# Performance work log

Measured on AMD Instinct MI355X. Metric: run time of the kernel, lower is better.

## Reference

```python
import jax, jax.numpy as jnp
import numpy as np

B, N, F, R, H = 64, 128, 128, 64, 256
L = 3           # number of DTNN layers (hidden_dim=[256,256,256])
FC = 256        # fc_hidden_dim[0]
OUT = 1
SCALE = 0.05


def setup_inputs() -> dict:
    key = jax.random.key(0)
    ks = jax.random.split(key, 12)
    inp = {
        "x": jax.random.normal(ks[0], (B, N, F), dtype=jnp.float32),
        # RBF-expanded pairwise distances are nonnegative
        "distance": jax.random.uniform(ks[1], (B, N, N, R), dtype=jnp.float32),
        # stacked per-layer params (all layers share shapes since hidden dims equal)
        "Wcf_w": jax.random.normal(ks[2], (L, H, F), dtype=jnp.float32) * SCALE,
        "Wcf_b": jax.random.normal(ks[3], (L, H), dtype=jnp.float32) * SCALE,
        "Wdf_w": jax.random.normal(ks[4], (L, H, R), dtype=jnp.float32) * SCALE,
        "Wdf_b": jax.random.normal(ks[5], (L, H), dtype=jnp.float32) * SCALE,
        "Wfc_w": jax.random.normal(ks[6], (L, F, H), dtype=jnp.float32) * SCALE,  # no bias
        "fc0_w": jax.random.normal(ks[7], (FC, F), dtype=jnp.float32) * SCALE,
        "fc0_b": jax.random.normal(ks[8], (FC,), dtype=jnp.float32) * SCALE,
        "out_w": jax.random.normal(ks[9], (OUT, FC), dtype=jnp.float32) * SCALE,
        "out_b": jax.random.normal(ks[10], (OUT,), dtype=jnp.float32) * SCALE,
    }
    return inp


def reference(x, distance, Wcf_w, Wcf_b, Wdf_w, Wdf_b, Wfc_w, fc0_w, fc0_b, out_w, out_b):
    # Original per-layer math:
    #   msg_i = sum_j Wfc( Wcf(x_i) * Wdf(d_ij) )
    # Since Wcf(x_i) is independent of j and all maps are linear, this equals
    #   Wfc( Wcf(x_i) * (sum_j d_ij) @ Wdf_w^T + N * Wdf_b ),
    # which avoids materializing the (B,N,N,H) grid while computing identical math.
    n = x.shape[1]
    d_sum = jnp.sum(distance, axis=2)  # (B, N, R)
    for l in range(Wcf_w.shape[0]):
        cf = jnp.einsum('bnf,hf->bnh', x, Wcf_w[l]) + Wcf_b[l]            # (B,N,H)
        df = jnp.einsum('bnr,hr->bnh', d_sum, Wdf_w[l]) + n * Wdf_b[l]    # (B,N,H)
        h = jnp.einsum('bnh,fh->bnf', cf * df, Wfc_w[l])                  # (B,N,F)
        x = h + jnp.tanh(h)                                                # residual-tanh
    g = jnp.sum(x, axis=1)                     # sum pooling over nodes -> (B,F)
    g = g @ fc0_w.T + fc0_b                    # (B,FC)
    return g @ out_w.T + out_b                 # (B,OUT)
```

## Files before the change

### kernel.cpp

```cpp
#include <hip/hip_runtime.h>
#include <math.h>

#define B_ 64
#define N_ 128
#define F_ 128
#define R_ 64
#define H_ 256
#define L_ 3
#define M_ (B_*N_)

#define DS_PAD 72
#define X_PAD 136
#define P_PAD 264

#define PREPW_NBLK 48
#define COMB_BID   48
#define DSUM_BID0  49

typedef short bf16x8 __attribute__((ext_vector_type(8)));
typedef float f32x4 __attribute__((ext_vector_type(4)));

__device__ __forceinline__ unsigned short f2bf(float f) {
    unsigned int u = __float_as_uint(f);
    u += 0x7FFF + ((u >> 16) & 1);
    return (unsigned short)(u >> 16);
}

__device__ __forceinline__ float tanh_fast(float h) {
    float a = fabsf(h);
    float e = __expf(-2.0f * a);
    float t = (1.0f - e) * __builtin_amdgcn_rcpf(1.0f + e);
    return copysignf(t, h);
}

__global__ __launch_bounds__(256)
void dsum_prep_kernel(const float* __restrict__ dist,
                      const float* __restrict__ wcf,
                      const float* __restrict__ wdf,
                      const float* __restrict__ wfc,
                      const float* __restrict__ fc0_w, const float* __restrict__ fc0_b,
                      const float* __restrict__ out_w, const float* __restrict__ out_b,
                      unsigned short* __restrict__ wcfb,
                      unsigned short* __restrict__ wdfb,
                      unsigned short* __restrict__ wfcb,
                      float* __restrict__ wcomb,
                      unsigned short* __restrict__ dsumb,
                      float* __restrict__ out) {
    const int bid = blockIdx.x;
    const int t   = threadIdx.x;

    if (bid < PREPW_NBLK) {
        const int NCF = L_*H_*F_/4;
        const int NDF = L_*H_*R_/4;
        const int NFC = L_*F_*H_/4;
        const int total = NCF + NDF + NFC;
        for (int i = bid*256 + t; i < total; i += PREPW_NBLK*256) {
            const float4* src; unsigned short* dst; int k;
            if (i < NCF)           { src = (const float4*)wcf; dst = wcfb; k = i; }
            else if (i < NCF+NDF)  { src = (const float4*)wdf; dst = wdfb; k = i-NCF; }
            else                   { src = (const float4*)wfc; dst = wfcb; k = i-NCF-NDF; }
            float4 v = src[k];
            ushort4 o; o.x=f2bf(v.x); o.y=f2bf(v.y); o.z=f2bf(v.z); o.w=f2bf(v.w);
            ((ushort4*)dst)[k] = o;
        }
        return;
    }
    if (bid == COMB_BID) {
        if (t < 128) {
            float s = 0.f;
            #pragma unroll 8
            for (int c = 0; c < 256; ++c) s += out_w[c] * fc0_w[c*128 + t];
            wcomb[t] = s;
        } else if (t < 192) {
            float bb = out_b[0];
            #pragma unroll 8
            for (int c = 0; c < 256; ++c) bb += out_w[c] * fc0_b[c];
            out[t - 128] = bb;
        }
        return;
    }

    const int row = bid - DSUM_BID0;
    const float4* src = (const float4*)(dist + (size_t)row * (N_*R_));
    const int q = t & 15, jg = t >> 4;
    float4 a = make_float4(0.f,0.f,0.f,0.f);
    #pragma unroll
    for (int j0 = 0; j0 < N_; j0 += 16) {
        float4 v = src[(j0 + jg)*16 + q];
        a.x += v.x; a.y += v.y; a.z += v.z; a.w += v.w;
    }
    __shared__ float4 sh[256];
    sh[t] = a;
    __syncthreads();
    if (t < 16) {
        float4 s = sh[t];
        for (int g = 1; g < 16; ++g) {
            float4 v = sh[t + 16*g];
            s.x += v.x; s.y += v.y; s.z += v.z; s.w += v.w;
        }
        ushort4 o; o.x=f2bf(s.x); o.y=f2bf(s.y); o.z=f2bf(s.z); o.w=f2bf(s.w);
        ((ushort4*)(dsumb + (size_t)row * R_))[t] = o;
    }
}

__global__ __launch_bounds__(512)
void layers_kernel(const float* __restrict__ x,
                   const unsigned short* __restrict__ dsumb,
                   const unsigned short* __restrict__ wcfb,
                   const unsigned short* __restrict__ wdfb,
                   const unsigned short* __restrict__ wfcb,
                   const float* __restrict__ bcf,
                   const float* __restrict__ bdf,
                   const float* __restrict__ wcomb,
                   float* __restrict__ out) {
    __shared__ __align__(16) unsigned short ds_lds[32][DS_PAD];
    __shared__ __align__(16) unsigned short x_lds[32][X_PAD];
    __shared__ __align__(16) unsigned short p_lds[32][P_PAD];

    const int blk  = blockIdx.x;
    const int t    = threadIdx.x;
    const int w    = t >> 6, lane = t & 63;
    const int lr   = lane & 15, lg = lane >> 4;
    const int mh   = w & 1,  nq = w >> 1;

    {
        const int row16 = t >> 4, q = t & 15;
        const float4* xs = (const float4*)(x + (size_t)(blk*32 + row16)*F_ + q*8);
        float4 xv0 = xs[0], xv1 = xs[1];
        bf16x8 xb;
        xb[0]=f2bf(xv0.x); xb[1]=f2bf(xv0.y); xb[2]=f2bf(xv0.z); xb[3]=f2bf(xv0.w);
        xb[4]=f2bf(xv1.x); xb[5]=f2bf(xv1.y); xb[6]=f2bf(xv1.z); xb[7]=f2bf(xv1.w);
        *(bf16x8*)&x_lds[row16][q*8] = xb;

        if (t < 256) {
            const uint4* dsrc = (const uint4*)(dsumb + (size_t)(blk*32 + (t>>3))*R_);
            uint4 v = dsrc[t & 7];
            *(uint4*)&ds_lds[t>>3][(t&7)*8] = v;
        }
    }
    __syncthreads();

    float pool_acc = 0.f;

    #pragma unroll 1
    for (int l = 0; l < L_; ++l) {
        const unsigned short* wcf = wcfb + l*H_*F_;
        const unsigned short* wdf = wdfb + l*H_*R_;
        const unsigned short* wfc = wfcb + l*F_*H_;

        bf16x8 xa[4], da[2];
        #pragma unroll
        for (int kc = 0; kc < 4; ++kc)
            xa[kc] = *(const bf16x8*)&x_lds[mh*16 + lr][kc*32 + lg*8];
        #pragma unroll
        for (int kc = 0; kc < 2; ++kc)
            da[kc] = *(const bf16x8*)&ds_lds[mh*16 + lr][kc*32 + lg*8];

        #pragma unroll
        for (int nt = 0; nt < 4; ++nt) {
            const int ncol = nq*64 + nt*16 + lr;
            f32x4 acf = {0.f,0.f,0.f,0.f}, adf = {0.f,0.f,0.f,0.f};
            #pragma unroll
            for (int kc = 0; kc < 4; ++kc) {
                bf16x8 b = *(const bf16x8*)(wcf + (size_t)ncol*F_ + kc*32 + lg*8);
                acf = __builtin_amdgcn_mfma_f32_16x16x32_bf16(xa[kc], b, acf, 0, 0, 0);
            }
            #pragma unroll
            for (int kc = 0; kc < 2; ++kc) {
                bf16x8 b = *(const bf16x8*)(wdf + (size_t)ncol*R_ + kc*32 + lg*8);
                adf = __builtin_amdgcn_mfma_f32_16x16x32_bf16(da[kc], b, adf, 0, 0, 0);
            }
            const float bc = bcf[l*H_ + ncol];
            const float bd = bdf[l*H_ + ncol] * 128.0f;
            #pragma unroll
            for (int j = 0; j < 4; ++j) {
                float p = (acf[j] + bc) * (adf[j] + bd);
                p_lds[mh*16 + lg*4 + j][ncol] = f2bf(p);
            }
        }
        __syncthreads();

        f32x4 ah[2] = {{0,0,0,0},{0,0,0,0}};
        #pragma unroll
        for (int kc = 0; kc < 8; ++kc) {
            bf16x8 ap = *(const bf16x8*)&p_lds[mh*16 + lr][kc*32 + lg*8];
            #pragma unroll
            for (int ct = 0; ct < 2; ++ct) {
                const int ncol = nq*32 + ct*16 + lr;
                bf16x8 b = *(const bf16x8*)(wfc + (size_t)ncol*H_ + kc*32 + lg*8);
                ah[ct] = __builtin_amdgcn_mfma_f32_16x16x32_bf16(ap, b, ah[ct], 0, 0, 0);
            }
        }
        __syncthreads();

        if (l < L_-1) {
            #pragma unroll
            for (int ct = 0; ct < 2; ++ct) {
                #pragma unroll
                for (int j = 0; j < 4; ++j) {
                    float h = ah[ct][j];
                    float xo = h + tanh_fast(h);
                    x_lds[mh*16 + lg*4 + j][nq*32 + ct*16 + lr] = f2bf(xo);
                }
            }
            __syncthreads();
        } else {
            #pragma unroll
            for (int ct = 0; ct < 2; ++ct) {
                const float wc = wcomb[nq*32 + ct*16 + lr];
                #pragma unroll
                for (int j = 0; j < 4; ++j) {
                    float h = ah[ct][j];
                    float xo = h + tanh_fast(h);
                    pool_acc += xo * wc;
                }
            }
        }
    }

    float* red = (float*)&p_lds[0][0];
    red[t] = pool_acc;
    __syncthreads();
    #pragma unroll
    for (int s = 256; s > 0; s >>= 1) {
        if (t < s) red[t] += red[t + s];
        __syncthreads();
    }
    if (t == 0) atomicAdd(&out[blk >> 2], red[0]);
}

extern "C" void kernel_launch(void* const* d_in, const int* in_sizes, int n_in,
                              void* d_out, int out_size, void* d_ws, size_t ws_size,
                              hipStream_t stream) {
    const float* x     = (const float*)d_in[0];
    const float* dist  = (const float*)d_in[1];
    const float* wcf_w = (const float*)d_in[2];
    const float* wcf_b = (const float*)d_in[3];
    const float* wdf_w = (const float*)d_in[4];
    const float* wdf_b = (const float*)d_in[5];
    const float* wfc_w = (const float*)d_in[6];
    const float* fc0_w = (const float*)d_in[7];
    const float* fc0_b = (const float*)d_in[8];
    const float* out_w = (const float*)d_in[9];
    const float* out_b = (const float*)d_in[10];
    float* out = (float*)d_out;

    char* ws = (char*)d_ws;
    unsigned short* wcfb  = (unsigned short*)(ws);
    unsigned short* wdfb  = (unsigned short*)(ws + 196608u);
    unsigned short* wfcb  = (unsigned short*)(ws + 294912u);
    float*          wcomb = (float*)(ws + 491520u);
    unsigned short* dsumb = (unsigned short*)(ws + 492032u);

    dsum_prep_kernel<<<DSUM_BID0 + M_, 256, 0, stream>>>(
        dist, wcf_w, wdf_w, wfc_w, fc0_w, fc0_b, out_w, out_b,
        wcfb, wdfb, wfcb, wcomb, dsumb, out);

    layers_kernel<<<M_/32, 512, 0, stream>>>(x, dsumb, wcfb, wdfb, wfcb,
                                             wcf_b, wdf_b, wcomb, out);
}
```

Baseline: 78.31 us.

## Fuse distance summation into layers kernel with 16-row blocks

Moves the per-row reduction over the 256 MB distance tensor out of the prep kernel and into the main layers kernel. Each of the 8 waves now sums two rows with shuffles, and the block tile shrinks from 32 to 16 rows so 512 blocks are launched. This removes the bf16 dsum round trip through global memory and lets the dominant distance read overlap with the MFMA layer compute. The cost is that weights are re-read by twice as many blocks, and the prep kernel now only converts weights, so it is tiny.

Result: slower. 88.86 us (+13.5%).

```diff
diff --git a/kernel.cpp b/kernel.cpp
--- a/kernel.cpp
+++ b/kernel.cpp
@@ -8,6 +8,8 @@
 #define H_ 256
 #define L_ 3
 #define M_ (B_*N_)
+#define RPB 16
+#define NBLK (M_/RPB)
 
 #define DS_PAD 72
 #define X_PAD 136
@@ -15,7 +17,6 @@
 
 #define PREPW_NBLK 48
 #define COMB_BID   48
-#define DSUM_BID0  49
 
 typedef short bf16x8 __attribute__((ext_vector_type(8)));
 typedef float f32x4 __attribute__((ext_vector_type(4)));
@@ -34,18 +35,16 @@
 }
 
 __global__ __launch_bounds__(256)
-void dsum_prep_kernel(const float* __restrict__ dist,
-                      const float* __restrict__ wcf,
-                      const float* __restrict__ wdf,
-                      const float* __restrict__ wfc,
-                      const float* __restrict__ fc0_w, const float* __restrict__ fc0_b,
-                      const float* __restrict__ out_w, const float* __restrict__ out_b,
-                      unsigned short* __restrict__ wcfb,
-                      unsigned short* __restrict__ wdfb,
-                      unsigned short* __restrict__ wfcb,
-                      float* __restrict__ wcomb,
-                      unsigned short* __restrict__ dsumb,
-                      float* __restrict__ out) {
+void prep_kernel(const float* __restrict__ wcf,
+                 const float* __restrict__ wdf,
+                 const float* __restrict__ wfc,
+                 const float* __restrict__ fc0_w, const float* __restrict__ fc0_b,
+                 const float* __restrict__ out_w, const float* __restrict__ out_b,
+                 unsigned short* __restrict__ wcfb,
+                 unsigned short* __restrict__ wdfb,
+                 unsigned short* __restrict__ wfcb,
+                 float* __restrict__ wcomb,
+                 float* __restrict__ out) {
     const int bid = blockIdx.x;
     const int t   = threadIdx.x;
 
@@ -65,77 +64,76 @@
         }
         return;
     }
-    if (bid == COMB_BID) {
-        if (t < 128) {
-            float s = 0.f;
-            #pragma unroll 8
-            for (int c = 0; c < 256; ++c) s += out_w[c] * fc0_w[c*128 + t];
-            wcomb[t] = s;
-        } else if (t < 192) {
-            float bb = out_b[0];
-            #pragma unroll 8
-            for (int c = 0; c < 256; ++c) bb += out_w[c] * fc0_b[c];
-            out[t - 128] = bb;
-        }
-        return;
-    }
-
-    const int row = bid - DSUM_BID0;
-    const float4* src = (const float4*)(dist + (size_t)row * (N_*R_));
-    const int q = t & 15, jg = t >> 4;
-    float4 a = make_float4(0.f,0.f,0.f,0.f);
-    #pragma unroll
-    for (int j0 = 0; j0 < N_; j0 += 16) {
-        float4 v = src[(j0 + jg)*16 + q];
-        a.x += v.x; a.y += v.y; a.z += v.z; a.w += v.w;
-    }
-    __shared__ float4 sh[256];
-    sh[t] = a;
-    __syncthreads();
-    if (t < 16) {
-        float4 s = sh[t];
-        for (int g = 1; g < 16; ++g) {
-            float4 v = sh[t + 16*g];
-            s.x += v.x; s.y += v.y; s.z += v.z; s.w += v.w;
-        }
-        ushort4 o; o.x=f2bf(s.x); o.y=f2bf(s.y); o.z=f2bf(s.z); o.w=f2bf(s.w);
-        ((ushort4*)(dsumb + (size_t)row * R_))[t] = o;
-    }
-}
-
-__global__ __launch_bounds__(512)
-void layers_kernel(const float* __restrict__ x,
-                   const unsigned short* __restrict__ dsumb,
-                   const unsigned short* __restrict__ wcfb,
-                   const unsigned short* __restrict__ wdfb,
-                   const unsigned short* __restrict__ wfcb,
-                   const float* __restrict__ bcf,
-                   const float* __restrict__ bdf,
-                   const float* __restrict__ wcomb,
-                   float* __restrict__ out) {
-    __shared__ __align__(16) unsigned short ds_lds[32][DS_PAD];
-    __shared__ __align__(16) unsigned short x_lds[32][X_PAD];
-    __shared__ __align__(16) unsigned short p_lds[32][P_PAD];
+    if (t < 128) {
+        float s = 0.f;
+        #pragma unroll 8
+        for (int c = 0; c < 256; ++c) s += out_w[c] * fc0_w[c*128 + t];
+        wcomb[t] = s;
+    } else if (t < 192) {
+        float bb = out_b[0];
+        #pragma unroll 8
+        for (int c = 0; c < 256; ++c) bb += out_w[c] * fc0_b[c];
+        out[t - 128] = bb;
+    }
+}
+
+__global__ __launch_bounds__(512, 4)
+void mega_kernel(const float* __restrict__ x,
+                 const float* __restrict__ dist,
+                 const unsigned short* __restrict__ wcfb,
+                 const unsigned short* __restrict__ wdfb,
+                 const unsigned short* __restrict__ wfcb,
+                 const float* __restrict__ biascf,
+                 const float* __restrict__ biasdf,
+                 const float* __restrict__ wcomb,
+                 float* __restrict__ out) {
+    __shared__ __align__(16) unsigned short ds_lds[RPB][DS_PAD];
+    __shared__ __align__(16) unsigned short x_lds[RPB][X_PAD];
+    __shared__ __align__(16) unsigned short p_lds[RPB][P_PAD];
 
     const int blk  = blockIdx.x;
     const int t    = threadIdx.x;
     const int w    = t >> 6, lane = t & 63;
     const int lr   = lane & 15, lg = lane >> 4;
-    const int mh   = w & 1,  nq = w >> 1;
 
     {
-        const int row16 = t >> 4, q = t & 15;
-        const float4* xs = (const float4*)(x + (size_t)(blk*32 + row16)*F_ + q*8);
-        float4 xv0 = xs[0], xv1 = xs[1];
-        bf16x8 xb;
-        xb[0]=f2bf(xv0.x); xb[1]=f2bf(xv0.y); xb[2]=f2bf(xv0.z); xb[3]=f2bf(xv0.w);
-        xb[4]=f2bf(xv1.x); xb[5]=f2bf(xv1.y); xb[6]=f2bf(xv1.z); xb[7]=f2bf(xv1.w);
-        *(bf16x8*)&x_lds[row16][q*8] = xb;
-
-        if (t < 256) {
-            const uint4* dsrc = (const uint4*)(dsumb + (size_t)(blk*32 + (t>>3))*R_);
-            uint4 v = dsrc[t & 7];
-            *(uint4*)&ds_lds[t>>3][(t&7)*8] = v;
+        const int row = t >> 5, c = t & 31;
+        float4 v = ((const float4*)(x + (size_t)(blk*RPB + row)*F_))[c];
+        ushort4 o; o.x=f2bf(v.x); o.y=f2bf(v.y); o.z=f2bf(v.z); o.w=f2bf(v.w);
+        *(ushort4*)&x_lds[row][c*4] = o;
+    }
+
+    {
+        const float4* s0 = (const float4*)(dist + (size_t)(blk*RPB + w*2) * (N_*R_));
+        const float4* s1 = s0 + (N_*R_/4);
+        float4 a00 = {0,0,0,0}, a01 = {0,0,0,0}, a10 = {0,0,0,0}, a11 = {0,0,0,0};
+        #pragma unroll 4
+        for (int ii = 0; ii < 32; ii += 2) {
+            float4 v0 = s0[ii*64 + lane];
+            float4 v1 = s0[(ii+1)*64 + lane];
+            float4 v2 = s1[ii*64 + lane];
+            float4 v3 = s1[(ii+1)*64 + lane];
+            a00.x+=v0.x; a00.y+=v0.y; a00.z+=v0.z; a00.w+=v0.w;
+            a01.x+=v1.x; a01.y+=v1.y; a01.z+=v1.z; a01.w+=v1.w;
+            a10.x+=v2.x; a10.y+=v2.y; a10.z+=v2.z; a10.w+=v2.w;
+            a11.x+=v3.x; a11.y+=v3.y; a11.z+=v3.z; a11.w+=v3.w;
+        }
+        float4 a0, a1;
+        a0.x=a00.x+a01.x; a0.y=a00.y+a01.y; a0.z=a00.z+a01.z; a0.w=a00.w+a01.w;
+        a1.x=a10.x+a11.x; a1.y=a10.y+a11.y; a1.z=a10.z+a11.z; a1.w=a10.w+a11.w;
+        a0.x += __shfl_xor(a0.x, 16); a0.y += __shfl_xor(a0.y, 16);
+        a0.z += __shfl_xor(a0.z, 16); a0.w += __shfl_xor(a0.w, 16);
+        a0.x += __shfl_xor(a0.x, 32); a0.y += __shfl_xor(a0.y, 32);
+        a0.z += __shfl_xor(a0.z, 32); a0.w += __shfl_xor(a0.w, 32);
+        a1.x += __shfl_xor(a1.x, 16); a1.y += __shfl_xor(a1.y, 16);
+        a1.z += __shfl_xor(a1.z, 16); a1.w += __shfl_xor(a1.w, 16);
+        a1.x += __shfl_xor(a1.x, 32); a1.y += __shfl_xor(a1.y, 32);
+        a1.z += __shfl_xor(a1.z, 32); a1.w += __shfl_xor(a1.w, 32);
+        if (lane < 16) {
+            ushort4 o0; o0.x=f2bf(a0.x); o0.y=f2bf(a0.y); o0.z=f2bf(a0.z); o0.w=f2bf(a0.w);
+            *(ushort4*)&ds_lds[w*2][lane*4] = o0;
+            ushort4 o1; o1.x=f2bf(a1.x); o1.y=f2bf(a1.y); o1.z=f2bf(a1.z); o1.w=f2bf(a1.w);
+            *(ushort4*)&ds_lds[w*2+1][lane*4] = o1;
         }
     }
     __syncthreads();
@@ -151,14 +149,14 @@
         bf16x8 xa[4], da[2];
         #pragma unroll
         for (int kc = 0; kc < 4; ++kc)
-            xa[kc] = *(const bf16x8*)&x_lds[mh*16 + lr][kc*32 + lg*8];
+            xa[kc] = *(const bf16x8*)&x_lds[lr][kc*32 + lg*8];
         #pragma unroll
         for (int kc = 0; kc < 2; ++kc)
-            da[kc] = *(const bf16x8*)&ds_lds[mh*16 + lr][kc*32 + lg*8];
-
-        #pragma unroll
-        for (int nt = 0; nt < 4; ++nt) {
-            const int ncol = nq*64 + nt*16 + lr;
+            da[kc] = *(const bf16x8*)&ds_lds[lr][kc*32 + lg*8];
+
+        #pragma unroll
+        for (int nt = 0; nt < 2; ++nt) {
+            const int ncol = w*32 + nt*16 + lr;
             f32x4 acf = {0.f,0.f,0.f,0.f}, adf = {0.f,0.f,0.f,0.f};
             #pragma unroll
             for (int kc = 0; kc < 4; ++kc) {
@@ -170,50 +168,40 @@
                 bf16x8 b = *(const bf16x8*)(wdf + (size_t)ncol*R_ + kc*32 + lg*8);
                 adf = __builtin_amdgcn_mfma_f32_16x16x32_bf16(da[kc], b, adf, 0, 0, 0);
             }
-            const float bc = bcf[l*H_ + ncol];
-            const float bd = bdf[l*H_ + ncol] * 128.0f;
+            const float bc = biascf[l*H_ + ncol];
+            const float bd = biasdf[l*H_ + ncol] * 128.0f;
             #pragma unroll
             for (int j = 0; j < 4; ++j) {
                 float p = (acf[j] + bc) * (adf[j] + bd);
-                p_lds[mh*16 + lg*4 + j][ncol] = f2bf(p);
+                p_lds[lg*4 + j][ncol] = f2bf(p);
             }
         }
         __syncthreads();
 
-        f32x4 ah[2] = {{0,0,0,0},{0,0,0,0}};
+        const int ncol2 = w*16 + lr;
+        f32x4 ah = {0.f,0.f,0.f,0.f};
         #pragma unroll
         for (int kc = 0; kc < 8; ++kc) {
-            bf16x8 ap = *(const bf16x8*)&p_lds[mh*16 + lr][kc*32 + lg*8];
-            #pragma unroll
-            for (int ct = 0; ct < 2; ++ct) {
-                const int ncol = nq*32 + ct*16 + lr;
-                bf16x8 b = *(const bf16x8*)(wfc + (size_t)ncol*H_ + kc*32 + lg*8);
-                ah[ct] = __builtin_amdgcn_mfma_f32_16x16x32_bf16(ap, b, ah[ct], 0, 0, 0);
-            }
+            bf16x8 b  = *(const bf16x8*)(wfc + (size_t)ncol2*H_ + kc*32 + lg*8);
+            bf16x8 ap = *(const bf16x8*)&p_lds[lr][kc*32 + lg*8];
+            ah = __builtin_amdgcn_mfma_f32_16x16x32_bf16(ap, b, ah, 0, 0, 0);
         }
         __syncthreads();
 
         if (l < L_-1) {
             #pragma unroll
-            for (int ct = 0; ct < 2; ++ct) {
-                #pragma unroll
-                for (int j = 0; j < 4; ++j) {
-                    float h = ah[ct][j];
-                    float xo = h + tanh_fast(h);
-                    x_lds[mh*16 + lg*4 + j][nq*32 + ct*16 + lr] = f2bf(xo);
-                }
+            for (int j = 0; j < 4; ++j) {
+                float h = ah[j];
+                float xo = h + tanh_fast(h);
+                x_lds[lg*4 + j][ncol2] = f2bf(xo);
             }
             __syncthreads();
         } else {
-            #pragma unroll
-            for (int ct = 0; ct < 2; ++ct) {
-                const float wc = wcomb[nq*32 + ct*16 + lr];
-                #pragma unroll
-                for (int j = 0; j < 4; ++j) {
-                    float h = ah[ct][j];
-                    float xo = h + tanh_fast(h);
-                    pool_acc += xo * wc;
-                }
+            const float wc = wcomb[ncol2];
+            #pragma unroll
+            for (int j = 0; j < 4; ++j) {
+                float h = ah[j];
+                pool_acc += (h + tanh_fast(h)) * wc;
             }
         }
     }
@@ -226,7 +214,7 @@
         if (t < s) red[t] += red[t + s];
         __syncthreads();
     }
-    if (t == 0) atomicAdd(&out[blk >> 2], red[0]);
+    if (t == 0) atomicAdd(&out[blk >> 3], red[0]);
 }
 
 extern "C" void kernel_launch(void* const* d_in, const int* in_sizes, int n_in,
@@ -250,12 +238,11 @@
     unsigned short* wdfb  = (unsigned short*)(ws + 196608u);
     unsigned short* wfcb  = (unsigned short*)(ws + 294912u);
     float*          wcomb = (float*)(ws + 491520u);
-    unsigned short* dsumb = (unsigned short*)(ws + 492032u);
-
-    dsum_prep_kernel<<<DSUM_BID0 + M_, 256, 0, stream>>>(
-        dist, wcf_w, wdf_w, wfc_w, fc0_w, fc0_b, out_w, out_b,
-        wcfb, wdfb, wfcb, wcomb, dsumb, out);
-
-    layers_kernel<<<M_/32, 512, 0, stream>>>(x, dsumb, wcfb, wdfb, wfcb,
-                                             wcf_b, wdf_b, wcomb, out);
-}
+
+    prep_kernel<<<COMB_BID + 1, 256, 0, stream>>>(
+        wcf_w, wdf_w, wfc_w, fc0_w, fc0_b, out_w, out_b,
+        wcfb, wdfb, wfcb, wcomb, out);
+
+    mega_kernel<<<NBLK, 512, 0, stream>>>(x, dist, wcfb, wdfb, wfcb,
+                                          wcf_b, wdf_b, wcomb, out);
+}
```
